# Kernel tuning notes

Measured on AMD Instinct MI355X. Metric: run time of the kernel, lower is better.

## Reference

```python
import jax, jax.numpy as jnp
import numpy as np

B, N, E, Dh, L = 64, 128, 1024, 300, 2  # batch, num_utter, emb_dim, hidden_dim, gnn_layers


def gru_cell(x, h, wih, whh, bih, bhh):
    # torch.nn.GRUCell math; gate order r, z, n
    gi = x @ wih.T + bih
    gh = h @ whh.T + bhh
    ir, iz, inn = jnp.split(gi, 3, axis=-1)
    hr, hz, hn = jnp.split(gh, 3, axis=-1)
    r = jax.nn.sigmoid(ir + hr)
    z = jax.nn.sigmoid(iz + hz)
    n = jnp.tanh(inn + r * hn)
    return (1.0 - z) * n + z * h


def dag_layer(Hl, mask, wg, bg, cwih, cwhh, cbih, cbhh, pwih, pwhh, pbih, pbhh):
    # Hl: (B,N,Dh); mask: (B,N,N) strict-causal DAG adjacency (float 0/1)
    wq, wk = wg[:Dh], wg[Dh:]  # GatLinear: Linear(2*Dh, 1) split over [Q; K]
    x0 = Hl[:, 0]
    z0 = jnp.zeros_like(x0)
    C0 = gru_cell(x0, z0, cwih, cwhh, cbih, cbhh)  # grus_c(H0, hx=None)
    P0 = gru_cell(z0, x0, pwih, pwhh, pbih, pbhh)  # grus_p(M=0, H0)
    buf0 = jnp.zeros_like(Hl).at[:, 0].set(C0 + P0)

    xs = (jnp.swapaxes(Hl[:, 1:], 0, 1),      # (N-1,B,Dh)
          jnp.swapaxes(mask[:, 1:], 0, 1),    # (N-1,B,N)
          jnp.arange(1, Hl.shape[1]))

    def step(buf, inp):
        x, m, i = inp  # x:(B,Dh), m:(B,N) allows only positions j<i with adj==1
        alpha = (x @ wq)[:, None] + buf @ wk + bg        # (B,N) additive score
        alpha = alpha - (1.0 - m) * 1e30                 # mask_logic
        w = jax.nn.softmax(alpha, axis=-1)
        M = jnp.einsum('bn,bnd->bd', w, buf)             # attn_sum over history H1
        C = gru_cell(x, M, cwih, cwhh, cbih, cbhh)       # grus_c(H_i, M)
        P = gru_cell(M, x, pwih, pwhh, pbih, pbhh)       # grus_p(M, H_i)
        return buf.at[:, i].set(C + P), None

    buf, _ = jax.lax.scan(step, buf0, xs)
    return buf


def setup_inputs():
    key = jax.random.key(0)
    ks = jax.random.split(key, 16)
    features = jax.random.normal(ks[0], (B, N, E), jnp.float32)
    adj = jax.random.randint(ks[1], (B, N, N), 0, 2, dtype=jnp.int32)
    idx = jnp.arange(1, N)
    adj = adj.at[:, idx, idx - 1].set(1)  # every utterance links to its predecessor (valid DAG)
    s_mask = jax.random.randint(ks[2], (B, N, N), 0, 2, dtype=jnp.int32)
    s_mask_onehot = jax.nn.one_hot(s_mask, 2, dtype=jnp.int32)
    lengths = jnp.full((B,), N, dtype=jnp.int32)
    s = 0.05
    return {
        'features': features,
        'fc1_w': jax.random.normal(ks[3], (E, Dh), jnp.float32) * s,
        'fc1_b': jnp.zeros((Dh,), jnp.float32),
        'gat_w': jax.random.normal(ks[4], (L, 2 * Dh), jnp.float32) * s,
        'gat_b': jnp.zeros((L,), jnp.float32),
        'gc_wih': jax.random.normal(ks[5], (L, 3 * Dh, Dh), jnp.float32) * s,
        'gc_whh': jax.random.normal(ks[6], (L, 3 * Dh, Dh), jnp.float32) * s,
        'gc_bih': jnp.zeros((L, 3 * Dh), jnp.float32),
        'gc_bhh': jnp.zeros((L, 3 * Dh), jnp.float32),
        'gp_wih': jax.random.normal(ks[7], (L, 3 * Dh, Dh), jnp.float32) * s,
        'gp_whh': jax.random.normal(ks[8], (L, 3 * Dh, Dh), jnp.float32) * s,
        'gp_bih': jnp.zeros((L, 3 * Dh), jnp.float32),
        'gp_bhh': jnp.zeros((L, 3 * Dh), jnp.float32),
        'adj': adj,
        's_mask': s_mask,
        's_mask_onehot': s_mask_onehot,
        'lengths': lengths,
    }


def reference(features, fc1_w, fc1_b, gat_w, gat_b, gc_wih, gc_whh, gc_bih, gc_bhh,
              gp_wih, gp_whh, gp_bih, gp_bhh, adj, s_mask, s_mask_onehot, lengths):
    H0 = jax.nn.relu(features @ fc1_w + fc1_b)                 # (B,N,Dh)
    causal = jnp.tril(jnp.ones((N, N), features.dtype), k=-1)  # strictly past (j<i)
    mask = adj.astype(features.dtype) * causal                 # adj[:, i, :i]
    Hs = [H0]
    Hl = H0
    for l in range(L):
        Hl = dag_layer(Hl, mask, gat_w[l], gat_b[l],
                       gc_wih[l], gc_whh[l], gc_bih[l], gc_bhh[l],
                       gp_wih[l], gp_whh[l], gp_bih[l], gp_bhh[l])
        Hs.append(Hl)
    Hs.append(features)
    # nodal_att_type=None -> attentive_node_features is identity; module returns H
    return jnp.concatenate(Hs, axis=2)  # (B,N,Dh*(L+1)+E)
```

## Files before the change

### kernel.cpp

```cpp
#include <hip/hip_runtime.h>
#include <hip/hip_fp16.h>

#define B_   64
#define NB   128
#define E_   1024
#define DH   300
#define G3   900
#define OUTD 1924
#define SLICES 4
#define PK_STRIDE 1800
#define MROW 160

typedef _Float16 h2raw __attribute__((ext_vector_type(2)));

__device__ __forceinline__ float dot2f(unsigned int m2, unsigned int w, float acc) {
    h2raw a, b;
    __builtin_memcpy(&a, &m2, 4);
    __builtin_memcpy(&b, &w, 4);
    return __builtin_amdgcn_fdot2(a, b, acc, false);
}

__device__ __forceinline__ unsigned int packh2(float x, float y) {
    __half2 h;
    h.x = __float2half_rn(x);
    h.y = __float2half_rn(y);
    unsigned int u;
    __builtin_memcpy(&u, &h, 4);
    return u;
}

__device__ __forceinline__ float sigmoidf_(float x) { return 1.f / (1.f + __expf(-x)); }
__device__ __forceinline__ float tanh_fast(float x) { return 1.f - 2.f / (__expf(2.f * x) + 1.f); }

__global__ __launch_bounds__(256)
void copy_feat(const float* __restrict__ f, float* __restrict__ out) {
    const long id = (long)blockIdx.x * 256 + threadIdx.x;
    const long r = id >> 8;
    const int  c = (int)(id & 255);
    const float4 v = ((const float4*)(f + r * E_))[c];
    ((float4*)(out + r * OUTD + 3 * DH))[c] = v;
}

__global__ __launch_bounds__(256)
void pack2(const float* __restrict__ gc_whh, const float* __restrict__ gp_wih,
           unsigned int* __restrict__ dst) {
    const int id = blockIdx.x * 256 + threadIdx.x;
    if (id >= 2 * 150 * PK_STRIDE) return;
    const int l   = id / (150 * PK_STRIDE);
    const int rem = id % (150 * PK_STRIDE);
    const int kp  = rem / PK_STRIDE;
    const int R   = rem % PK_STRIDE;
    const int mat = R / G3;
    const int o   = R % G3;
    const float* W = (mat ? gp_wih : gc_whh) + (long)l * G3 * DH;
    const float2 v = *(const float2*)(W + (long)o * DH + 2 * kp);
    dst[id] = packh2(v.x, v.y);
}

__global__ __launch_bounds__(256)
void pack_af(const float* __restrict__ src, unsigned int* __restrict__ dst) {
    const long id = (long)blockIdx.x * 256 + threadIdx.x;
    const long r = id >> 9;
    const int kp = (int)(id & 511);
    const float2 v = *(const float2*)(src + r * E_ + 2 * kp);
    dst[id] = packh2(v.x, v.y);
}

__global__ __launch_bounds__(256)
void pack_ah(const float* __restrict__ src, unsigned int* __restrict__ dst) {
    const long id = (long)blockIdx.x * 256 + threadIdx.x;
    const long r = id / 160;
    const int kp = (int)(id % 160);
    unsigned int u = 0u;
    if (kp < 150) {
        const float2 v = *(const float2*)(src + r * OUTD + 2 * kp);
        u = packh2(v.x, v.y);
    }
    dst[id] = u;
}

__global__ __launch_bounds__(256)
void pack_bf(const float* __restrict__ W, unsigned int* __restrict__ dst) {
    const int id = blockIdx.x * 256 + threadIdx.x;
    const int n = id >> 9;
    const int kp = id & 511;
    unsigned int u = 0u;
    if (n < DH) u = packh2(W[(2 * kp) * DH + n], W[(2 * kp + 1) * DH + n]);
    dst[id] = u;
}

__global__ __launch_bounds__(256)
void pack_bw(const float* __restrict__ W, unsigned int* __restrict__ dst) {
    const int id = blockIdx.x * 256 + threadIdx.x;
    const int n = id / 160;
    const int kp = id % 160;
    unsigned int u = 0u;
    if (n < G3 && kp < 150) {
        const float2 v = *(const float2*)(W + (long)n * DH + 2 * kp);
        u = packh2(v.x, v.y);
    }
    dst[id] = u;
}

template<int RELU>
__global__ __launch_bounds__(256)
void gemm_h16(const unsigned int* __restrict__ APK, int ldap,
              const unsigned int* __restrict__ BPK, int ldbp,
              const float* __restrict__ bias,
              float* __restrict__ C, int ldc,
              int N, int KP)
{
    __shared__ __align__(16) unsigned int As[16][132];
    __shared__ __align__(16) unsigned int Bs[16][68];
    const int tid = threadIdx.x;
    const int m0 = blockIdx.y * 128;
    const int n0 = blockIdx.x * 64;
    const int tx = tid & 15, ty = tid >> 4;
    const int am = tid >> 1, ak8 = (tid & 1) * 8;
    const int bn = tid >> 2, bk4 = (tid & 3) * 4;

    float acc[8][4] = {{0.f}};
    const unsigned int* ap = APK + (long)(m0 + am) * ldap + ak8;
    const unsigned int* bp = BPK + (long)(n0 + bn) * ldbp + bk4;

    for (int kp0 = 0; kp0 < KP; kp0 += 16) {
        const uint4 a0 = *(const uint4*)(ap + kp0);
        const uint4 a1 = *(const uint4*)(ap + kp0 + 4);
        const uint4 bq = *(const uint4*)(bp + kp0);
        As[ak8 + 0][am] = a0.x; As[ak8 + 1][am] = a0.y;
        As[ak8 + 2][am] = a0.z; As[ak8 + 3][am] = a0.w;
        As[ak8 + 4][am] = a1.x; As[ak8 + 5][am] = a1.y;
        As[ak8 + 6][am] = a1.z; As[ak8 + 7][am] = a1.w;
        Bs[bk4 + 0][bn] = bq.x; Bs[bk4 + 1][bn] = bq.y;
        Bs[bk4 + 2][bn] = bq.z; Bs[bk4 + 3][bn] = bq.w;
        __syncthreads();
        #pragma unroll
        for (int kp = 0; kp < 16; ++kp) {
            const uint4 aA = *(const uint4*)&As[kp][ty * 8];
            const uint4 aB = *(const uint4*)&As[kp][ty * 8 + 4];
            const uint4 bb = *(const uint4*)&Bs[kp][tx * 4];
            const unsigned int av[8] = {aA.x, aA.y, aA.z, aA.w, aB.x, aB.y, aB.z, aB.w};
            const unsigned int bv[4] = {bb.x, bb.y, bb.z, bb.w};
            #pragma unroll
            for (int ii = 0; ii < 8; ++ii)
                #pragma unroll
                for (int jj = 0; jj < 4; ++jj)
                    acc[ii][jj] = dot2f(av[ii], bv[jj], acc[ii][jj]);
        }
        __syncthreads();
    }

    const int gn0 = n0 + tx * 4;
    #pragma unroll
    for (int ii = 0; ii < 8; ++ii) {
        const int gm = m0 + ty * 8 + ii;
        float* cp = C + (long)gm * ldc + gn0;
        if (gn0 + 3 < N) {
            const float4 bb = *(const float4*)&bias[gn0];
            float4 o;
            o.x = acc[ii][0] + bb.x; o.y = acc[ii][1] + bb.y;
            o.z = acc[ii][2] + bb.z; o.w = acc[ii][3] + bb.w;
            if (RELU) { o.x = fmaxf(o.x, 0.f); o.y = fmaxf(o.y, 0.f); o.z = fmaxf(o.z, 0.f); o.w = fmaxf(o.w, 0.f); }
            *(float4*)cp = o;
        } else if (gn0 < N) {
            for (int jj = 0; jj < 4; ++jj) {
                const int gn = gn0 + jj;
                if (gn < N) {
                    float v = acc[ii][jj] + bias[gn];
                    if (RELU) v = fmaxf(v, 0.f);
                    cp[jj] = v;
                }
            }
        }
    }
}

__global__ __launch_bounds__(512, 2)
void scan9(float* __restrict__ out,
           const float* __restrict__ GIC,
           const float* __restrict__ GHP,
           const unsigned int* __restrict__ PK2L,
           const float* __restrict__ cbhh,
           const float* __restrict__ pbih,
           const int* __restrict__ adj,
           const float* __restrict__ wk,
           unsigned long long* __restrict__ TBL,
           int l)
{
    extern __shared__ unsigned int histp[];
    __shared__ float wsm2[NB];
    __shared__ float betas[NB];
    __shared__ float Mlds[DH];
    __shared__ __align__(16) unsigned int M2[152];
    __shared__ float gmv[456];
    __shared__ float mx2s, S_pres;

    const int tid = threadIdx.x;
    const int lane = tid & 63;
    const int wid = tid >> 6;
    const int b = blockIdx.x & 63;
    const int k = blockIdx.x >> 6;
    const int swk = (k == 3) ? 72 : 76;

    float* outb = out + (long)b * NB * OUTD;
    const float* xcol = outb + l * DH;
    float* ycol = outb + (l + 1) * DH;
    const float* gicb = GIC + (long)b * NB * G3;
    const float* ghpb = GHP + (long)b * NB * G3;
    const int* adjb = adj + b * NB * NB;
    unsigned long long* mb = TBL + (long)b * NB * MROW;
    unsigned int* mb32 = (unsigned int*)mb;

    if (tid < 152) M2[tid] = 0u;

    const int D = 76 * k + ((tid < swk) ? tid : 0);
    const float cb0 = cbhh[D], cb1 = cbhh[DH + D], cb2 = cbhh[2 * DH + D];
    const float pb0 = pbih[D], pb1 = pbih[DH + D], pb2 = pbih[2 * DH + D];
    const float wkD = wk[D];

    const int ROWS = 6 * swk;
    int R;
    {
        const int t = (tid < ROWS) ? tid : 0;
        const int d = t % swk;
        const int r = t / swk;
        R = (r / 3) * G3 + (r % 3) * DH + 76 * k + d;
    }
    unsigned int w[152];
    #pragma unroll
    for (int j = 0; j < 150; ++j) w[j] = PK2L[j * PK_STRIDE + R];
    w[150] = 0u; w[151] = 0u;

    __syncthreads();

    const bool isv = (tid >= 256) && (tid < 406);
    const int vt = tid - 256;

    for (int i = 0; i < NB; ++i) {
        float gi0 = 0, gi1 = 0, gi2 = 0, gp0 = 0, gp1 = 0, gp2 = 0, xi = 0;
        if (tid < swk) {
            const float* gic = gicb + (long)i * G3;
            const float* ghp = ghpb + (long)i * G3;
            gi0 = gic[D]; gi1 = gic[DH + D]; gi2 = gic[2 * DH + D];
            gp0 = ghp[D]; gp1 = ghp[DH + D]; gp2 = ghp[2 * DH + D];
            xi = xcol[(long)i * OUTD + D];
        }
        int a0p = 0, a1p = 0;
        if (wid == 2 && i + 1 < NB) {
            a0p = adjb[(i + 1) * NB + lane];
            a1p = adjb[(i + 1) * NB + 64 + lane];
        }

        if (i > 0) {
            float V0 = 0.f, V1 = 0.f;
            if (wid == 0) {
                const unsigned long long* trow = mb + (long)(i - 1) * MROW;
                const unsigned int tag = (unsigned int)i;
                const bool act = (lane < 8);
                unsigned long long tv = 0;
                while (true) {
                    if (act && (unsigned int)tv != tag)
                        tv = __hip_atomic_load(&trow[152 + lane],
                                               __ATOMIC_RELAXED, __HIP_MEMORY_SCOPE_AGENT);
                    if (__all(!act || (unsigned int)tv == tag)) break;
                }
                float bp = 0.f;
                if (act) {
                    const unsigned int hb = (unsigned int)(tv >> 32);
                    __builtin_memcpy(&bp, &hb, 4);
                }
                bp += __shfl_xor(bp, 1);
                bp += __shfl_xor(bp, 2);
                bp += __shfl_xor(bp, 4);
                if (lane == 0) betas[i - 1] = __shfl(bp, 0);

                unsigned long long d0 = 0, d1 = 0;
                if (lane < 38) {
                    d0 = __hip_atomic_load(&trow[2 * lane],
                                           __ATOMIC_RELAXED, __HIP_MEMORY_SCOPE_AGENT);
                    d1 = __hip_atomic_load(&trow[2 * lane + 1],
                                           __ATOMIC_RELAXED, __HIP_MEMORY_SCOPE_AGENT);
                    uint4 q;
                    q.x = (unsigned int)d0; q.y = (unsigned int)(d0 >> 32);
                    q.z = (unsigned int)d1; q.w = (unsigned int)(d1 >> 32);
                    *(uint4*)&histp[(i - 1) * 152 + 4 * lane] = q;
                }
            } else if (isv) {
                #pragma unroll 4
                for (int j = 0; j + 1 < i; ++j) {
                    const float wj = wsm2[j];
                    const unsigned int u = histp[j * 152 + vt];
                    __half2 h; __builtin_memcpy(&h, &u, 4);
                    V0 = fmaf(wj, __half2float(h.x), V0);
                    V1 = fmaf(wj, __half2float(h.y), V1);
                }
            }
            __syncthreads();

            if (isv) {
                const float beta_new = betas[i - 1];
                const float mxl = mx2s;
                float S = S_pres, e;
                if (beta_new > mxl) {
                    const float sc = __expf(mxl - beta_new);
                    V0 *= sc; V1 *= sc; S *= sc; e = 1.f;
                } else {
                    e = __expf(beta_new - mxl);
                }
                const unsigned int u = histp[(i - 1) * 152 + vt];
                __half2 h; __builtin_memcpy(&h, &u, 4);
                S += e;
                V0 = fmaf(e, __half2float(h.x), V0);
                V1 = fmaf(e, __half2float(h.y), V1);
                const float inv = 1.f / S;
                const float m0 = V0 * inv, m1 = V1 * inv;
                Mlds[2 * vt] = m0;
                Mlds[2 * vt + 1] = m1;
                M2[vt] = packh2(m0, m1);
            }
        } else {
            if (tid < DH) Mlds[tid] = 0.f;
        }
        __syncthreads();

        if (tid < ROWS) {
            float a0 = 0.f, a1 = 0.f;
            #pragma unroll
            for (int j4 = 0; j4 < 152; j4 += 4) {
                const uint4 m4 = *(const uint4*)&M2[j4];
                a0 = dot2f(m4.x, w[j4 + 0], a0);
                a1 = dot2f(m4.y, w[j4 + 1], a1);
                a0 = dot2f(m4.z, w[j4 + 2], a0);
                a1 = dot2f(m4.w, w[j4 + 3], a1);
            }
            gmv[tid] = a0 + a1;
        }
        __syncthreads();

        if (wid < 2) {
            float rowv = 0.f;
            if (tid < swk) {
                const float Mi = Mlds[D];
                const float hc0 = gmv[0 * swk + tid] + cb0;
                const float hc1 = gmv[1 * swk + tid] + cb1;
                const float hc2 = gmv[2 * swk + tid] + cb2;
                const float rc = sigmoidf_(gi0 + hc0);
                const float zc = sigmoidf_(gi1 + hc1);
                const float nc = tanh_fast(gi2 + rc * hc2);
                const float Cc = (1.f - zc) * nc + zc * Mi;
                const float ip0 = gmv[3 * swk + tid] + pb0;
                const float ip1 = gmv[4 * swk + tid] + pb1;
                const float ip2 = gmv[5 * swk + tid] + pb2;
                const float rp = sigmoidf_(ip0 + gp0);
                const float zp = sigmoidf_(ip1 + gp1);
                const float np = tanh_fast(ip2 + rp * gp2);
                const float Pp = (1.f - zp) * np + zp * xi;
                rowv = Cc + Pp;
            }
            const float pr = __shfl_xor(rowv, 1);
            const unsigned int pairu32 = packh2(rowv, pr);
            if (tid < swk && !(tid & 1)) {
                __hip_atomic_store(&mb32[(long)i * (MROW * 2) + 38 * k + (tid >> 1)], pairu32,
                                   __ATOMIC_RELAXED, __HIP_MEMORY_SCOPE_AGENT);
            }
            float bv = (tid < swk) ? rowv * wkD : 0.f;
            #pragma unroll
            for (int off = 32; off; off >>= 1) bv += __shfl_xor(bv, off);
            asm volatile("s_waitcnt vmcnt(0)" ::: "memory");
            if (lane == 0) {
                unsigned int bbits;
                __builtin_memcpy(&bbits, &bv, 4);
                const unsigned long long pkt =
                    ((unsigned long long)bbits << 32) | (unsigned int)(i + 1);
                __hip_atomic_store(&mb[(long)i * MROW + 152 + 2 * k + wid], pkt,
                                   __ATOMIC_RELAXED, __HIP_MEMORY_SCOPE_AGENT);
            }
            if (tid < swk) ycol[(long)i * OUTD + D] = rowv;
        } else if (wid == 2 && i + 1 < NB) {
            const int j1 = lane + 64;
            const bool v0 = (lane < i) && (a0p != 0);
            const bool v1 = (j1 < i) && (a1p != 0);
            const float aa0 = v0 ? betas[lane] : -3.0e38f;
            const float aa1 = v1 ? betas[j1]   : -3.0e38f;
            float mx = fmaxf(aa0, aa1);
            #pragma unroll
            for (int off = 32; off; off >>= 1) mx = fmaxf(mx, __shfl_xor(mx, off));
            const float e0 = v0 ? __expf(aa0 - mx) : 0.f;
            const float e1 = v1 ? __expf(aa1 - mx) : 0.f;
            float s = e0 + e1;
            #pragma unroll
            for (int off = 32; off; off >>= 1) s += __shfl_xor(s, off);
            wsm2[lane] = e0;
            wsm2[j1]   = e1;
            if (lane == 0) { mx2s = mx; S_pres = s; }
        }
        __syncthreads();
    }
}

extern "C" void kernel_launch(void* const* d_in, const int* in_sizes, int n_in,
                              void* d_out, int out_size, void* d_ws, size_t ws_size,
                              hipStream_t stream) {
    (void)in_sizes; (void)n_in; (void)out_size; (void)ws_size;
    const float* features = (const float*)d_in[0];
    const float* fc1_w    = (const float*)d_in[1];
    const float* fc1_b    = (const float*)d_in[2];
    const float* gat_w    = (const float*)d_in[3];
    const float* gc_wih   = (const float*)d_in[5];
    const float* gc_whh   = (const float*)d_in[6];
    const float* gc_bih   = (const float*)d_in[7];
    const float* gc_bhh   = (const float*)d_in[8];
    const float* gp_wih   = (const float*)d_in[9];
    const float* gp_whh   = (const float*)d_in[10];
    const float* gp_bih   = (const float*)d_in[11];
    const float* gp_bhh   = (const float*)d_in[12];
    const int*   adj      = (const int*)d_in[13];
    float* out = (float*)d_out;

    unsigned long long* TB = (unsigned long long*)d_ws;
    float* GIC = (float*)(TB + 2L * B_ * NB * MROW);
    float* GHP = GIC + (long)B_ * NB * G3;
    unsigned int* PK2  = (unsigned int*)(GHP + (long)B_ * NB * G3);
    unsigned int* APK2 = PK2 + 2 * 150 * PK_STRIDE;
    unsigned int* BPKF = APK2 + 8192L * 160;
    unsigned int* BPKL = BPKF + 320L * 512;
    unsigned int* APK1 = (unsigned int*)GIC;

    hipFuncSetAttribute(reinterpret_cast<const void*>(scan9),
                        hipFuncAttributeMaxDynamicSharedMemorySize, 80000);
    hipMemsetAsync(TB, 0, 2L * B_ * NB * MROW * sizeof(unsigned long long), stream);

    copy_feat<<<dim3((B_ * NB * E_) / 1024), 256, 0, stream>>>(features, out);
    pack2<<<dim3((2 * 150 * PK_STRIDE + 255) / 256), 256, 0, stream>>>(gc_whh, gp_wih, PK2);

    pack_af<<<dim3(8192 * 512 / 256), 256, 0, stream>>>(features, APK1);
    pack_bf<<<dim3(320 * 512 / 256), 256, 0, stream>>>(fc1_w, BPKF);
    pack_bw<<<dim3(960 * 160 / 256), 256, 0, stream>>>(gc_wih,               BPKL + 0L * 153600);
    pack_bw<<<dim3(960 * 160 / 256), 256, 0, stream>>>(gp_whh,               BPKL + 1L * 153600);
    pack_bw<<<dim3(960 * 160 / 256), 256, 0, stream>>>(gc_wih + G3 * DH,     BPKL + 2L * 153600);
    pack_bw<<<dim3(960 * 160 / 256), 256, 0, stream>>>(gp_whh + G3 * DH,     BPKL + 3L * 153600);

    gemm_h16<1><<<dim3(5, 64), 256, 0, stream>>>(APK1, 512, BPKF, 512, fc1_b, out, OUTD, DH, 512);

    for (int l = 0; l < 2; ++l) {
        pack_ah<<<dim3(8192 * 160 / 256), 256, 0, stream>>>(out + l * DH, APK2);
        gemm_h16<0><<<dim3(15, 64), 256, 0, stream>>>(
            APK2, 160, BPKL + (2L * l) * 153600, 160, gc_bih + l * G3, GIC, G3, G3, 160);
        gemm_h16<0><<<dim3(15, 64), 256, 0, stream>>>(
            APK2, 160, BPKL + (2L * l + 1) * 153600, 160, gp_bhh + l * G3, GHP, G3, G3, 160);
        scan9<<<dim3(SLICES * B_), 512, 77824, stream>>>(
            out, GIC, GHP, PK2 + (long)l * 150 * PK_STRIDE,
            gc_bhh + l * G3, gp_bih + l * G3, adj,
            gat_w + l * 2 * DH + DH,
            TB + (long)l * B_ * NB * MROW, l);
    }
}
```

Before: 1.218 ms.

## Fuse per-layer input GEMMs and emit fp16-packed activations from producers

Merges the two per-layer input-projection GEMMs (grus_c input and grus_p hidden) into one GEMM over a concatenated 1800-row weight matrix with split bias, writing a single interleaved GG buffer. The pack_ah kernel is removed: the fc1 GEMM writes fp16-packed output directly, and the layer-0 scan writes its packed row pairs into APK2 for layer 1. The four weight-pack launches become one, and the scan's tag-wait path issues its row loads before the beta reduction. This is meant to cut kernel launches and extra passes over activations, at the cost of an extra memset and a larger GEMM grid.

```diff
diff --git a/kernel.cpp b/kernel.cpp
--- a/kernel.cpp
+++ b/kernel.cpp
@@ -6,10 +6,12 @@
 #define E_   1024
 #define DH   300
 #define G3   900
+#define G6   1800
 #define OUTD 1924
 #define SLICES 4
 #define PK_STRIDE 1800
 #define MROW 160
+#define BROWS 1856
 
 typedef _Float16 h2raw __attribute__((ext_vector_type(2)));
 
@@ -67,19 +69,6 @@
 }
 
 __global__ __launch_bounds__(256)
-void pack_ah(const float* __restrict__ src, unsigned int* __restrict__ dst) {
-    const long id = (long)blockIdx.x * 256 + threadIdx.x;
-    const long r = id / 160;
-    const int kp = (int)(id % 160);
-    unsigned int u = 0u;
-    if (kp < 150) {
-        const float2 v = *(const float2*)(src + r * OUTD + 2 * kp);
-        u = packh2(v.x, v.y);
-    }
-    dst[id] = u;
-}
-
-__global__ __launch_bounds__(256)
 void pack_bf(const float* __restrict__ W, unsigned int* __restrict__ dst) {
     const int id = blockIdx.x * 256 + threadIdx.x;
     const int n = id >> 9;
@@ -90,24 +79,31 @@
 }
 
 __global__ __launch_bounds__(256)
-void pack_bw(const float* __restrict__ W, unsigned int* __restrict__ dst) {
+void pack_bw2(const float* __restrict__ Wc, const float* __restrict__ Wp,
+              unsigned int* __restrict__ dst) {
     const int id = blockIdx.x * 256 + threadIdx.x;
-    const int n = id / 160;
-    const int kp = id % 160;
+    if (id >= 2 * BROWS * 160) return;
+    const int l   = id / (BROWS * 160);
+    const int rem = id % (BROWS * 160);
+    const int n   = rem / 160;
+    const int kp  = rem % 160;
     unsigned int u = 0u;
-    if (n < G3 && kp < 150) {
-        const float2 v = *(const float2*)(W + (long)n * DH + 2 * kp);
+    if (n < G6 && kp < 150) {
+        const float* W = (n < G3 ? Wc : Wp) + (long)l * G3 * DH;
+        const int o = (n < G3) ? n : n - G3;
+        const float2 v = *(const float2*)(W + (long)o * DH + 2 * kp);
         u = packh2(v.x, v.y);
     }
     dst[id] = u;
 }
 
-template<int RELU>
+template<int RELU, int PACKOUT>
 __global__ __launch_bounds__(256)
 void gemm_h16(const unsigned int* __restrict__ APK, int ldap,
               const unsigned int* __restrict__ BPK, int ldbp,
-              const float* __restrict__ bias,
+              const float* __restrict__ bias1, const float* __restrict__ bias2, int bsplit,
               float* __restrict__ C, int ldc,
+              unsigned int* __restrict__ CPK, int ldcp,
               int N, int KP)
 {
     __shared__ __align__(16) unsigned int As[16][132];
@@ -156,17 +152,23 @@
         const int gm = m0 + ty * 8 + ii;
         float* cp = C + (long)gm * ldc + gn0;
         if (gn0 + 3 < N) {
-            const float4 bb = *(const float4*)&bias[gn0];
+            const float* bb4 = (gn0 < bsplit) ? bias1 + gn0 : bias2 + (gn0 - bsplit);
+            const float4 bb = *(const float4*)bb4;
             float4 o;
             o.x = acc[ii][0] + bb.x; o.y = acc[ii][1] + bb.y;
             o.z = acc[ii][2] + bb.z; o.w = acc[ii][3] + bb.w;
             if (RELU) { o.x = fmaxf(o.x, 0.f); o.y = fmaxf(o.y, 0.f); o.z = fmaxf(o.z, 0.f); o.w = fmaxf(o.w, 0.f); }
             *(float4*)cp = o;
+            if (PACKOUT) {
+                unsigned int* pk = CPK + (long)gm * ldcp + (gn0 >> 1);
+                pk[0] = packh2(o.x, o.y);
+                pk[1] = packh2(o.z, o.w);
+            }
         } else if (gn0 < N) {
             for (int jj = 0; jj < 4; ++jj) {
                 const int gn = gn0 + jj;
                 if (gn < N) {
-                    float v = acc[ii][jj] + bias[gn];
+                    float v = acc[ii][jj] + ((gn < bsplit) ? bias1[gn] : bias2[gn - bsplit]);
                     if (RELU) v = fmaxf(v, 0.f);
                     cp[jj] = v;
                 }
@@ -176,16 +178,16 @@
 }
 
 __global__ __launch_bounds__(512, 2)
-void scan9(float* __restrict__ out,
-           const float* __restrict__ GIC,
-           const float* __restrict__ GHP,
-           const unsigned int* __restrict__ PK2L,
-           const float* __restrict__ cbhh,
-           const float* __restrict__ pbih,
-           const int* __restrict__ adj,
-           const float* __restrict__ wk,
-           unsigned long long* __restrict__ TBL,
-           int l)
+void scan14(float* __restrict__ out,
+            const float* __restrict__ GG,
+            const unsigned int* __restrict__ PK2L,
+            const float* __restrict__ cbhh,
+            const float* __restrict__ pbih,
+            const int* __restrict__ adj,
+            const float* __restrict__ wk,
+            unsigned long long* __restrict__ TBL,
+            unsigned int* __restrict__ APKN,
+            int l)
 {
     extern __shared__ unsigned int histp[];
     __shared__ float wsm2[NB];
@@ -205,8 +207,7 @@
     float* outb = out + (long)b * NB * OUTD;
     const float* xcol = outb + l * DH;
     float* ycol = outb + (l + 1) * DH;
-    const float* gicb = GIC + (long)b * NB * G3;
-    const float* ghpb = GHP + (long)b * NB * G3;
+    const float* ggb = GG + (long)b * NB * G6;
     const int* adjb = adj + b * NB * NB;
     unsigned long long* mb = TBL + (long)b * NB * MROW;
     unsigned int* mb32 = (unsigned int*)mb;
@@ -239,10 +240,9 @@
     for (int i = 0; i < NB; ++i) {
         float gi0 = 0, gi1 = 0, gi2 = 0, gp0 = 0, gp1 = 0, gp2 = 0, xi = 0;
         if (tid < swk) {
-            const float* gic = gicb + (long)i * G3;
-            const float* ghp = ghpb + (long)i * G3;
+            const float* gic = ggb + (long)i * G6;
             gi0 = gic[D]; gi1 = gic[DH + D]; gi2 = gic[2 * DH + D];
-            gp0 = ghp[D]; gp1 = ghp[DH + D]; gp2 = ghp[2 * DH + D];
+            gp0 = gic[G3 + D]; gp1 = gic[G3 + DH + D]; gp2 = gic[G3 + 2 * DH + D];
             xi = xcol[(long)i * OUTD + D];
         }
         int a0p = 0, a1p = 0;
@@ -264,22 +264,24 @@
                                                __ATOMIC_RELAXED, __HIP_MEMORY_SCOPE_AGENT);
                     if (__all(!act || (unsigned int)tv == tag)) break;
                 }
-                float bp = 0.f;
-                if (act) {
-                    const unsigned int hb = (unsigned int)(tv >> 32);
-                    __builtin_memcpy(&bp, &hb, 4);
-                }
-                bp += __shfl_xor(bp, 1);
-                bp += __shfl_xor(bp, 2);
-                bp += __shfl_xor(bp, 4);
-                if (lane == 0) betas[i - 1] = __shfl(bp, 0);
-
                 unsigned long long d0 = 0, d1 = 0;
                 if (lane < 38) {
                     d0 = __hip_atomic_load(&trow[2 * lane],
                                            __ATOMIC_RELAXED, __HIP_MEMORY_SCOPE_AGENT);
                     d1 = __hip_atomic_load(&trow[2 * lane + 1],
                                            __ATOMIC_RELAXED, __HIP_MEMORY_SCOPE_AGENT);
+                }
+                float bp = 0.f;
+                if (act) {
+                    const unsigned int hb = (unsigned int)(tv >> 32);
+                    __builtin_memcpy(&bp, &hb, 4);
+                }
+                bp += __shfl_xor(bp, 1);
+                bp += __shfl_xor(bp, 2);
+                bp += __shfl_xor(bp, 4);
+                if (lane == 0) betas[i - 1] = __shfl(bp, 0);
+
+                if (lane < 38) {
                     uint4 q;
                     q.x = (unsigned int)d0; q.y = (unsigned int)(d0 >> 32);
                     q.z = (unsigned int)d1; q.w = (unsigned int)(d1 >> 32);
@@ -362,6 +364,8 @@
             if (tid < swk && !(tid & 1)) {
                 __hip_atomic_store(&mb32[(long)i * (MROW * 2) + 38 * k + (tid >> 1)], pairu32,
                                    __ATOMIC_RELAXED, __HIP_MEMORY_SCOPE_AGENT);
+                if (l == 0)
+                    APKN[((long)b * NB + i) * 160 + 38 * k + (tid >> 1)] = pairu32;
             }
             float bv = (tid < swk) ? rowv * wkD : 0.f;
             #pragma unroll
@@ -418,40 +422,38 @@
     float* out = (float*)d_out;
 
     unsigned long long* TB = (unsigned long long*)d_ws;
-    float* GIC = (float*)(TB + 2L * B_ * NB * MROW);
-    float* GHP = GIC + (long)B_ * NB * G3;
-    unsigned int* PK2  = (unsigned int*)(GHP + (long)B_ * NB * G3);
+    float* GG = (float*)(TB + 2L * B_ * NB * MROW);
+    unsigned int* PK2  = (unsigned int*)(GG + 8192L * G6);
     unsigned int* APK2 = PK2 + 2 * 150 * PK_STRIDE;
     unsigned int* BPKF = APK2 + 8192L * 160;
     unsigned int* BPKL = BPKF + 320L * 512;
-    unsigned int* APK1 = (unsigned int*)GIC;
-
-    hipFuncSetAttribute(reinterpret_cast<const void*>(scan9),
+    unsigned int* APK1 = (unsigned int*)GG;
+
+    hipFuncSetAttribute(reinterpret_cast<const void*>(scan14),
                         hipFuncAttributeMaxDynamicSharedMemorySize, 80000);
     hipMemsetAsync(TB, 0, 2L * B_ * NB * MROW * sizeof(unsigned long long), stream);
+    hipMemsetAsync(APK2, 0, 8192L * 160 * sizeof(unsigned int), stream);
 
     copy_feat<<<dim3((B_ * NB * E_) / 1024), 256, 0, stream>>>(features, out);
     pack2<<<dim3((2 * 150 * PK_STRIDE + 255) / 256), 256, 0, stream>>>(gc_whh, gp_wih, PK2);
 
     pack_af<<<dim3(8192 * 512 / 256), 256, 0, stream>>>(features, APK1);
     pack_bf<<<dim3(320 * 512 / 256), 256, 0, stream>>>(fc1_w, BPKF);
-    pack_bw<<<dim3(960 * 160 / 256), 256, 0, stream>>>(gc_wih,               BPKL + 0L * 153600);
-    pack_bw<<<dim3(960 * 160 / 256), 256, 0, stream>>>(gp_whh,               BPKL + 1L * 153600);
-    pack_bw<<<dim3(960 * 160 / 256), 256, 0, stream>>>(gc_wih + G3 * DH,     BPKL + 2L * 153600);
-    pack_bw<<<dim3(960 * 160 / 256), 256, 0, stream>>>(gp_whh + G3 * DH,     BPKL + 3L * 153600);
-
-    gemm_h16<1><<<dim3(5, 64), 256, 0, stream>>>(APK1, 512, BPKF, 512, fc1_b, out, OUTD, DH, 512);
+    pack_bw2<<<dim3((2 * BROWS * 160 + 255) / 256), 256, 0, stream>>>(gc_wih, gp_whh, BPKL);
+
+    gemm_h16<1, 1><<<dim3(5, 64), 256, 0, stream>>>(
+        APK1, 512, BPKF, 512, fc1_b, fc1_b, DH, out, OUTD, APK2, 160, DH, 512);
 
     for (int l = 0; l < 2; ++l) {
-        pack_ah<<<dim3(8192 * 160 / 256), 256, 0, stream>>>(out + l * DH, APK2);
-        gemm_h16<0><<<dim3(15, 64), 256, 0, stream>>>(
-            APK2, 160, BPKL + (2L * l) * 153600, 160, gc_bih + l * G3, GIC, G3, G3, 160);
-        gemm_h16<0><<<dim3(15, 64), 256, 0, stream>>>(
-            APK2, 160, BPKL + (2L * l + 1) * 153600, 160, gp_bhh + l * G3, GHP, G3, G3, 160);
-        scan9<<<dim3(SLICES * B_), 512, 77824, stream>>>(
-            out, GIC, GHP, PK2 + (long)l * 150 * PK_STRIDE,
+        gemm_h16<0, 0><<<dim3(29, 64), 256, 0, stream>>>(
+            APK2, 160, BPKL + (long)l * BROWS * 160, 160,
+            gc_bih + l * G3, gp_bhh + l * G3, G3,
+            GG, G6, (unsigned int*)nullptr, 0, G6, 160);
+        scan14<<<dim3(SLICES * B_), 512, 77824, stream>>>(
+            out, GG, PK2 + (long)l * 150 * PK_STRIDE,
             gc_bhh + l * G3, gp_bih + l * G3, adj,
             gat_w + l * 2 * DH + DH,
-            TB + (long)l * B_ * NB * MROW, l);
-    }
-}
+            TB + (long)l * B_ * NB * MROW,
+            APK2, l);
+    }
+}
```

Result: faster. 1.174 ms (-3.7%).
